# Kernel tuning notes

Hardware: AMD Instinct MI355X
Metric: run time of the kernel (lower is better)

## Reference

```python
import jax, jax.numpy as jnp
import numpy as np

NUM_HEADS = 16
HEAD_DIM = 64
D_MODEL = 1024
OUTPUT_DIM = 1024


def setup_inputs() -> dict:
    key = jax.random.key(0)
    ks = jax.random.split(key, 11)
    B, S, H = 2, 2048, D_MODEL
    inner = NUM_HEADS * HEAD_DIM
    s = 0.02
    return {
        "query": jax.random.normal(ks[0], (B, S, H), jnp.float32),
        "key": jax.random.normal(ks[1], (B, S, H), jnp.float32),
        "value": jax.random.normal(ks[2], (B, S, H), jnp.float32),
        "Wq": jax.random.normal(ks[3], (H, inner), jnp.float32) * s,
        "bq": jnp.zeros((inner,), jnp.float32),
        "Wk": jax.random.normal(ks[4], (H, inner), jnp.float32) * s,
        "bk": jnp.zeros((inner,), jnp.float32),
        "Wv": jax.random.normal(ks[5], (H, inner), jnp.float32) * s,
        "bv": jnp.zeros((inner,), jnp.float32),
        "Wo": jax.random.normal(ks[6], (inner, OUTPUT_DIM), jnp.float32) * s,
        "bo": jnp.zeros((OUTPUT_DIM,), jnp.float32),
    }


def reference(query, key, value, Wq, bq, Wk, bk, Wv, bv, Wo, bo):
    B, Sq, _ = query.shape
    Sk = key.shape[1]
    nh, dh = NUM_HEADS, HEAD_DIM
    # projections -> [B, S, nh, dh]
    Q = (query @ Wq + bq).reshape(B, Sq, nh, dh)
    K = (key @ Wk + bk).reshape(B, Sk, nh, dh)
    V = (value @ Wv + bv).reshape(B, Sk, nh, dh)
    # scores [B, nh, Sq, Sk]
    scores = jnp.einsum("bqhd,bkhd->bhqk", Q, K) / jnp.sqrt(jnp.float32(dh))
    attn = jax.nn.softmax(scores, axis=-1)
    out = jnp.einsum("bhqk,bkhd->bqhd", attn, V).reshape(B, Sq, nh * dh)
    return out @ Wo + bo
```

## Files before the change

### kernel.cpp

```cpp
#include <hip/hip_runtime.h>
#include <math.h>

typedef __attribute__((ext_vector_type(8))) short short8;
typedef __attribute__((ext_vector_type(4))) short short4v;
typedef __attribute__((ext_vector_type(4))) float f32x4;
typedef __attribute__((ext_vector_type(2))) float f32x2;

#if __has_builtin(__builtin_amdgcn_mfma_f32_16x16x16bf16_1k)
#define HAVE_MFMA16 1
#else
#define HAVE_MFMA16 0
#endif

__device__ __forceinline__ short f2bf(float f) {
  union { float f; unsigned u; } x; x.f = f;
  unsigned r = x.u + 0x7fffu + ((x.u >> 16) & 1u);
  return (short)(r >> 16);
}
#if __has_builtin(__builtin_amdgcn_cvt_pk_bf16_f32)
typedef __attribute__((ext_vector_type(2))) __bf16 bf16x2;
__device__ __forceinline__ unsigned pack_bf(float a, float b) {
  union { bf16x2 v; unsigned u; } t;
  t.v = __builtin_amdgcn_cvt_pk_bf16_f32(a, b);
  return t.u;
}
#else
__device__ __forceinline__ unsigned pack_bf(float a, float b) {
  union { float f; unsigned u; } x, y; x.f = a; y.f = b;
  unsigned ra = x.u + 0x7fffu + ((x.u >> 16) & 1u);
  unsigned rb = y.u + 0x7fffu + ((y.u >> 16) & 1u);
  return (ra >> 16) | (rb & 0xffff0000u);
}
#endif
__device__ __forceinline__ float fast_exp2(float x) {
#if __has_builtin(__builtin_amdgcn_exp2f)
  return __builtin_amdgcn_exp2f(x);
#else
  return exp2f(x);
#endif
}
union U4S8 { unsigned u[4]; short8 s; };
union U2S4 { unsigned u[2]; short4v s; };

__device__ __forceinline__ void async16(const short* g, short* lds_uniform) {
  __builtin_amdgcn_global_load_lds(
      (const __attribute__((address_space(1))) void*)g,
      (__attribute__((address_space(3))) void*)lds_uniform, 16, 0, 0);
}

__global__ __launch_bounds__(256) void wconv(
    const float* __restrict__ W0, const float* __restrict__ W1,
    const float* __restrict__ W2, const float* __restrict__ W3,
    short* __restrict__ T0, short* __restrict__ T1,
    short* __restrict__ T2, short* __restrict__ T3) {
  const float* W; short* T;
  switch (blockIdx.z) {
    case 0: W = W0; T = T0; break;
    case 1: W = W1; T = T1; break;
    case 2: W = W2; T = T2; break;
    default: W = W3; T = T3; break;
  }
  __shared__ __align__(16) short t[64][72];
  const int tid = threadIdx.x;
  const int x0 = blockIdx.x * 64, y0 = blockIdx.y * 64;
  {
    int rr = tid >> 2, cc = (tid & 3) * 16;
    const float* p = W + (size_t)(x0 + rr) * 1024 + y0 + cc;
    f32x4 v[4];
    v[0] = *(const f32x4*)(p + 0);  v[1] = *(const f32x4*)(p + 4);
    v[2] = *(const f32x4*)(p + 8);  v[3] = *(const f32x4*)(p + 12);
#pragma unroll
    for (int i = 0; i < 4; ++i)
#pragma unroll
      for (int j = 0; j < 4; ++j)
        t[cc + 4 * i + j][rr] = f2bf(v[i][j]);
  }
  __syncthreads();
  {
    int nr = tid >> 2, kc = (tid & 3) * 16;
    short* q = T + (size_t)(y0 + nr) * 1024 + x0 + kc;
    *(short8*)q       = *(const short8*)&t[nr][kc];
    *(short8*)(q + 8) = *(const short8*)&t[nr][kc + 8];
  }
}

__global__ __launch_bounds__(256) void aconv(
    const float* __restrict__ X0, const float* __restrict__ X1, const float* __restrict__ X2,
    short* __restrict__ Y0, short* __restrict__ Y1, short* __restrict__ Y2) {
  const float* X; short* Y;
  switch (blockIdx.z) {
    case 0: X = X0; Y = Y0; break;
    case 1: X = X1; Y = Y1; break;
    default: X = X2; Y = Y2; break;
  }
  size_t idx = ((size_t)blockIdx.x * 256 + threadIdx.x) * 16;
  f32x4 v0 = *(const f32x4*)(X + idx + 0);
  f32x4 v1 = *(const f32x4*)(X + idx + 4);
  f32x4 v2 = *(const f32x4*)(X + idx + 8);
  f32x4 v3 = *(const f32x4*)(X + idx + 12);
  U4S8 a, b;
  a.u[0] = pack_bf(v0[0], v0[1]); a.u[1] = pack_bf(v0[2], v0[3]);
  a.u[2] = pack_bf(v1[0], v1[1]); a.u[3] = pack_bf(v1[2], v1[3]);
  b.u[0] = pack_bf(v2[0], v2[1]); b.u[1] = pack_bf(v2[2], v2[3]);
  b.u[2] = pack_bf(v3[0], v3[1]); b.u[3] = pack_bf(v3[2], v3[3]);
  *(short8*)(Y + idx) = a.s;
  *(short8*)(Y + idx + 8) = b.s;
}

template <bool OUT_F32, int BM>
__global__ __launch_bounds__(256) void gemm_async(
    const short* __restrict__ A0, const short* __restrict__ A1, const short* __restrict__ A2,
    const short* __restrict__ B0, const short* __restrict__ B1, const short* __restrict__ B2,
    const float* __restrict__ b0, const float* __restrict__ b1, const float* __restrict__ b2,
    void* __restrict__ C0, void* __restrict__ C1, void* __restrict__ C2,
    float s0, float s1, float s2, int M, int N, int K) {
  const int z = blockIdx.z;
  const short* A    = z == 0 ? A0 : (z == 1 ? A1 : A2);
  const short* B    = z == 0 ? B0 : (z == 1 ? B1 : B2);
  const float* bias = z == 0 ? b0 : (z == 1 ? b1 : b2);
  void*        Cv   = z == 0 ? C0 : (z == 1 ? C1 : C2);
  const float  cs   = z == 0 ? s0 : (z == 1 ? s1 : s2);

  constexpr int MF = BM / 32;
  constexpr int AJ = BM / 64;
  __shared__ __align__(16) short As[BM * 32];
  __shared__ __align__(16) short Bs[128 * 32];
  const int tid = threadIdx.x;
  const int l = tid & 63, w = tid >> 6;
  const int lr = l & 15, lq = l >> 4;
  const int lin = blockIdx.x + (int)gridDim.x * blockIdx.y;
  const int ny = (int)gridDim.y;
  const int yb = lin % ny, xb = lin / ny;
  const int m0 = yb * BM, n0 = xb * 128;
  const int wm = (w >> 1) * (BM / 2), wn = (w & 1) * 64;
  f32x4 acc[MF][4] = {};

  const int lrow = l >> 2, lcol = (l & 3) * 8;
  const short* aptr[AJ];
  short* alds[AJ];
#pragma unroll
  for (int j = 0; j < AJ; ++j) {
    int chunk = w * AJ + j;
    aptr[j] = A + (size_t)(m0 + chunk * 16 + lrow) * K + lcol;
    alds[j] = &As[chunk * 512];
  }
  const short* bptr[2];
  short* blds[2];
#pragma unroll
  for (int j = 0; j < 2; ++j) {
    int chunk = w * 2 + j;
    bptr[j] = B + (size_t)(n0 + chunk * 16 + lrow) * K + lcol;
    blds[j] = &Bs[chunk * 512];
  }

  const int KT = K >> 5;
  for (int kt = 0; kt < KT; ++kt) {
    const int k0 = kt * 32;
    __syncthreads();
#pragma unroll
    for (int j = 0; j < AJ; ++j) async16(aptr[j] + k0, alds[j]);
#pragma unroll
    for (int j = 0; j < 2; ++j) async16(bptr[j] + k0, blds[j]);
    __syncthreads();

    short8 af[MF], bfr[4];
#pragma unroll
    for (int i = 0; i < MF; ++i)
      af[i] = *(const short8*)&As[(wm + i * 16 + lr) * 32 + lq * 8];
#pragma unroll
    for (int i = 0; i < 4; ++i)
      bfr[i] = *(const short8*)&Bs[(wn + i * 16 + lr) * 32 + lq * 8];
#pragma unroll
    for (int mi = 0; mi < MF; ++mi)
#pragma unroll
      for (int ni = 0; ni < 4; ++ni)
        acc[mi][ni] = __builtin_amdgcn_mfma_f32_16x16x32_bf16(af[mi], bfr[ni], acc[mi][ni], 0, 0, 0);
  }

#pragma unroll
  for (int ni = 0; ni < 4; ++ni) {
    int gn = n0 + wn + ni * 16 + lr;
    float bv = bias[gn];
#pragma unroll
    for (int mi = 0; mi < MF; ++mi) {
      int gm = m0 + wm + mi * 16 + lq * 4;
#pragma unroll
      for (int r = 0; r < 4; ++r) {
        float val = (acc[mi][ni][r] + bv) * cs;
        if constexpr (OUT_F32)
          ((float*)Cv)[(size_t)(gm + r) * N + gn] = val;
        else
          ((short*)Cv)[(size_t)(gm + r) * N + gn] = f2bf(val);
      }
    }
  }
}

template <bool A_IS_F32, bool B_IS_BF16, bool OUT_F32, int BM>
__global__ __launch_bounds__(256) void gemm_bias(
    const void* __restrict__ A0, const void* __restrict__ A1, const void* __restrict__ A2,
    const void* __restrict__ B0, const void* __restrict__ B1, const void* __restrict__ B2,
    const float* __restrict__ b0, const float* __restrict__ b1, const float* __restrict__ b2,
    void* __restrict__ C0, void* __restrict__ C1, void* __restrict__ C2,
    float s0, float s1, float s2, int M, int N, int K) {
  const int z = blockIdx.z;
  const void*  Av   = z == 0 ? A0 : (z == 1 ? A1 : A2);
  const void*  Bv   = z == 0 ? B0 : (z == 1 ? B1 : B2);
  const float* bias = z == 0 ? b0 : (z == 1 ? b1 : b2);
  void*        Cv   = z == 0 ? C0 : (z == 1 ? C1 : C2);
  const float  cs   = z == 0 ? s0 : (z == 1 ? s1 : s2);

  constexpr int MF = BM / 32;
  __shared__ __align__(16) short As[BM * 40];
  __shared__ __align__(16) short Bs[128 * 40];
  const int tid = threadIdx.x;
  const int l = tid & 63, w = tid >> 6;
  const int lr = l & 15, lq = l >> 4;
  const int lin = blockIdx.x + (int)gridDim.x * blockIdx.y;
  const int ny = (int)gridDim.y;
  const int yb = lin % ny, xb = lin / ny;
  const int m0 = yb * BM, n0 = xb * 128;
  const int wm = (w >> 1) * (BM / 2), wn = (w & 1) * 64;
  f32x4 acc[MF][4] = {};

  constexpr int TPR = 256 / BM;
  const int ar = tid / TPR, ac = (tid % TPR) * (32 / TPR);
  const int br = tid >> 1, bcc = (tid & 1) * 16;
  const int dp = tid & 63, kb = tid >> 6;

  f32x4 avf[MF];
  short8 avb[BM / 64 > 0 ? BM / 64 : 1];
  short8 bvb[2];
  f32x2 bvf[8];

  auto load_regs = [&](int k0) {
    if constexpr (A_IS_F32) {
      const float* Ap = (const float*)Av + (size_t)(m0 + ar) * K + k0 + ac;
#pragma unroll
      for (int i = 0; i < MF; ++i) avf[i] = *(const f32x4*)(Ap + 4 * i);
    } else {
      const short* Ap = (const short*)Av + (size_t)(m0 + ar) * K + k0 + ac;
#pragma unroll
      for (int i = 0; i < BM / 64; ++i) avb[i] = *(const short8*)(Ap + 8 * i);
    }
    if constexpr (B_IS_BF16) {
      const short* Bp = (const short*)Bv + (size_t)(n0 + br) * K + k0 + bcc;
      bvb[0] = *(const short8*)(Bp + 0);
      bvb[1] = *(const short8*)(Bp + 8);
    } else {
      const float* Bp = (const float*)Bv + (size_t)(k0 + kb * 8) * N + n0 + 2 * dp;
#pragma unroll
      for (int i = 0; i < 4; ++i) {
        bvf[2 * i]     = *(const f32x2*)(Bp + (size_t)(2 * i) * N);
        bvf[2 * i + 1] = *(const f32x2*)(Bp + (size_t)(2 * i + 1) * N);
      }
    }
  };
  auto write_lds = [&]() {
    if constexpr (A_IS_F32) {
#pragma unroll
      for (int j = 0; j < MF / 2; ++j) {
        U4S8 p;
        p.u[0] = pack_bf(avf[2 * j][0], avf[2 * j][1]);
        p.u[1] = pack_bf(avf[2 * j][2], avf[2 * j][3]);
        p.u[2] = pack_bf(avf[2 * j + 1][0], avf[2 * j + 1][1]);
        p.u[3] = pack_bf(avf[2 * j + 1][2], avf[2 * j + 1][3]);
        *(short8*)&As[ar * 40 + ac + 8 * j] = p.s;
      }
    } else {
#pragma unroll
      for (int j = 0; j < BM / 64; ++j)
        *(short8*)&As[ar * 40 + ac + 8 * j] = avb[j];
    }
    if constexpr (B_IS_BF16) {
      *(short8*)&Bs[br * 40 + bcc] = bvb[0];
      *(short8*)&Bs[br * 40 + bcc + 8] = bvb[1];
    } else {
      U4S8 lo, hi;
#pragma unroll
      for (int i = 0; i < 4; ++i) {
        lo.u[i] = pack_bf(bvf[2 * i][0], bvf[2 * i + 1][0]);
        hi.u[i] = pack_bf(bvf[2 * i][1], bvf[2 * i + 1][1]);
      }
      *(short8*)&Bs[(2 * dp) * 40 + kb * 8] = lo.s;
      *(short8*)&Bs[(2 * dp + 1) * 40 + kb * 8] = hi.s;
    }
  };

  load_regs(0);
  const int KT = K >> 5;
  for (int kt = 0; kt < KT; ++kt) {
    write_lds();
    __syncthreads();
    if (kt + 1 < KT) load_regs((kt + 1) * 32);

    short8 af[MF], bfr[4];
#pragma unroll
    for (int i = 0; i < MF; ++i)
      af[i] = *(const short8*)&As[(wm + i * 16 + lr) * 40 + lq * 8];
#pragma unroll
    for (int i = 0; i < 4; ++i)
      bfr[i] = *(const short8*)&Bs[(wn + i * 16 + lr) * 40 + lq * 8];
#pragma unroll
    for (int mi = 0; mi < MF; ++mi)
#pragma unroll
      for (int ni = 0; ni < 4; ++ni)
        acc[mi][ni] = __builtin_amdgcn_mfma_f32_16x16x32_bf16(af[mi], bfr[ni], acc[mi][ni], 0, 0, 0);
    __syncthreads();
  }

#pragma unroll
  for (int ni = 0; ni < 4; ++ni) {
    int gn = n0 + wn + ni * 16 + lr;
    float bv = bias[gn];
#pragma unroll
    for (int mi = 0; mi < MF; ++mi) {
      int gm = m0 + wm + mi * 16 + lq * 4;
#pragma unroll
      for (int r = 0; r < 4; ++r) {
        float val = (acc[mi][ni][r] + bv) * cs;
        if constexpr (OUT_F32)
          ((float*)Cv)[(size_t)(gm + r) * N + gn] = val;
        else
          ((short*)Cv)[(size_t)(gm + r) * N + gn] = f2bf(val);
      }
    }
  }
}

__global__ __launch_bounds__(256) void attn128db(
    const short* __restrict__ Q, const short* __restrict__ K,
    const short* __restrict__ V, short* __restrict__ ctx) {
  __shared__ __align__(16) short Ks[2][64][72];
  __shared__ __align__(16) short Vt[2][64][72];
#if !HAVE_MFMA16
  __shared__ __align__(16) short Ps2[4][32][68];
#endif
  const int tid = threadIdx.x, l = tid & 63, w = tid >> 6;
  const int lr = l & 15, lq = l >> 4;
  const int lin = blockIdx.x + 16 * blockIdx.y;
  const int h = lin & 15, qblk = lin >> 4;
  const int b = blockIdx.z, q0 = qblk * 128;
  const size_t bh = (size_t)b * 2048 * 1024 + (size_t)h * 64;
  const short* Kg = K + bh;
  const short* Vg = V + bh;

  short8 qb[2][2];
#pragma unroll
  for (int qf = 0; qf < 2; ++qf)
#pragma unroll
    for (int ks = 0; ks < 2; ++ks)
      qb[qf][ks] = *(const short8*)&Q[bh + (size_t)(q0 + w * 32 + qf * 16 + lr) * 1024 + ks * 32 + lq * 8];

  f32x4 accO[4][2] = {};
  float lpart[2] = {0.f, 0.f};

  const int kr = tid >> 2, kc = (tid & 3) * 16;
  const int vdp = tid & 31, vkb = tid >> 5;
  const int vswz = ((vkb + (vdp >> 2)) & 7) * 8;

  short8 kv0, kv1;
  unsigned vu[8];
  auto load_kv = [&](int kt) {
    const short* Kp = &Kg[(size_t)(kt * 64 + kr) * 1024 + kc];
    kv0 = *(const short8*)(Kp + 0);
    kv1 = *(const short8*)(Kp + 8);
#pragma unroll
    for (int i = 0; i < 8; ++i)
      vu[i] = *(const unsigned*)&Vg[(size_t)(kt * 64 + vkb * 8 + i) * 1024 + vdp * 2];
  };
  auto write_kv = [&](int buf) {
    *(short8*)&Ks[buf][kr][kc] = kv0;
    *(short8*)&Ks[buf][kr][kc + 8] = kv1;
    U4S8 lo, hi;
#pragma unroll
    for (int j = 0; j < 4; ++j) {
      lo.u[j] = (vu[2 * j] & 0xffffu) | (vu[2 * j + 1] << 16);
      hi.u[j] = (vu[2 * j] >> 16) | (vu[2 * j + 1] & 0xffff0000u);
    }
    *(short8*)&Vt[buf][2 * vdp][vswz] = lo.s;
    *(short8*)&Vt[buf][2 * vdp + 1][vswz] = hi.s;
  };

  load_kv(0);
  for (int kt = 0; kt < 32; ++kt) {
    const int buf = kt & 1;
    write_kv(buf);
    __syncthreads();
    if (kt + 1 < 32) load_kv(kt + 1);

    short8 ka[4][2];
#pragma unroll
    for (int ni = 0; ni < 4; ++ni)
#pragma unroll
      for (int ks = 0; ks < 2; ++ks)
        ka[ni][ks] = *(const short8*)&Ks[buf][ni * 16 + lr][ks * 32 + lq * 8];
    f32x4 s[4][2] = {};
#pragma unroll
    for (int ni = 0; ni < 4; ++ni)
#pragma unroll
      for (int qf = 0; qf < 2; ++qf) {
        s[ni][qf] = __builtin_amdgcn_mfma_f32_16x16x32_bf16(ka[ni][0], qb[qf][0], s[ni][qf], 0, 0, 0);
        s[ni][qf] = __builtin_amdgcn_mfma_f32_16x16x32_bf16(ka[ni][1], qb[qf][1], s[ni][qf], 0, 0, 0);
      }

    unsigned pk[4][2][2];
#pragma unroll
    for (int ni = 0; ni < 4; ++ni)
#pragma unroll
      for (int qf = 0; qf < 2; ++qf) {
        float p0 = fast_exp2(s[ni][qf][0]);
        float p1 = fast_exp2(s[ni][qf][1]);
        float p2 = fast_exp2(s[ni][qf][2]);
        float p3 = fast_exp2(s[ni][qf][3]);
        lpart[qf] += (p0 + p1) + (p2 + p3);
        pk[ni][qf][0] = pack_bf(p0, p1);
        pk[ni][qf][1] = pack_bf(p2, p3);
      }

#if HAVE_MFMA16
#pragma unroll
    for (int di = 0; di < 4; ++di) {
      const int dR = di * 16 + lr;
      const int ud = 2 * di + (lr >> 3);
#pragma unroll
      for (int ni = 0; ni < 4; ++ni) {
        const int pb = ((2 * ni + (lq >> 1) + ud) & 7) * 8 + (lq & 1) * 4;
        short4v vb = *(const short4v*)&Vt[buf][dR][pb];
#pragma unroll
        for (int qf = 0; qf < 2; ++qf) {
          U2S4 a; a.u[0] = pk[ni][qf][0]; a.u[1] = pk[ni][qf][1];
          accO[di][qf] = __builtin_amdgcn_mfma_f32_16x16x16bf16_1k(a.s, vb, accO[di][qf], 0, 0, 0);
        }
      }
    }
#else
#pragma unroll
    for (int ni = 0; ni < 4; ++ni)
#pragma unroll
      for (int qf = 0; qf < 2; ++qf) {
        unsigned* dst = (unsigned*)&Ps2[w][qf * 16 + lr][16 * ni + 4 * lq];
        dst[0] = pk[ni][qf][0];
        dst[1] = pk[ni][qf][1];
      }
#pragma unroll
    for (int ks = 0; ks < 2; ++ks)
#pragma unroll
      for (int qf = 0; qf < 2; ++qf) {
        const short* src = &Ps2[w][qf * 16 + lr][32 * ks + 8 * lq];
        U4S8 a;
        a.u[0] = ((const unsigned*)src)[0]; a.u[1] = ((const unsigned*)src)[1];
        a.u[2] = ((const unsigned*)src)[2]; a.u[3] = ((const unsigned*)src)[3];
#pragma unroll
        for (int di = 0; di < 4; ++di) {
          const int dR = di * 16 + lr;
          const int ud = 2 * di + (lr >> 3);
          const int pb = ((4 * ks + lq + ud) & 7) * 8;
          short8 vb = *(const short8*)&Vt[buf][dR][pb];
          accO[di][qf] = __builtin_amdgcn_mfma_f32_16x16x32_bf16(a.s, vb, accO[di][qf], 0, 0, 0);
        }
      }
#endif
  }

#pragma unroll
  for (int qf = 0; qf < 2; ++qf) {
    lpart[qf] += __shfl_xor(lpart[qf], 16, 64);
    lpart[qf] += __shfl_xor(lpart[qf], 32, 64);
  }
  float inv[2] = {1.0f / lpart[0], 1.0f / lpart[1]};
  float ir[2][4];
#pragma unroll
  for (int qf = 0; qf < 2; ++qf)
#pragma unroll
    for (int r = 0; r < 4; ++r)
      ir[qf][r] = __shfl(inv[qf], 4 * lq + r, 64);

#pragma unroll
  for (int qf = 0; qf < 2; ++qf)
#pragma unroll
    for (int r = 0; r < 4; ++r) {
      size_t row = bh + (size_t)(q0 + w * 32 + qf * 16 + 4 * lq + r) * 1024;
#pragma unroll
      for (int di = 0; di < 4; ++di)
        ctx[row + di * 16 + lr] = f2bf(accO[di][qf][r] * ir[qf][r]);
    }
}

extern "C" void kernel_launch(void* const* d_in, const int* in_sizes, int n_in,
                              void* d_out, int out_size, void* d_ws, size_t ws_size,
                              hipStream_t stream) {
  const void*  query = d_in[0];
  const void*  key   = d_in[1];
  const void*  value = d_in[2];
  const float* Wq = (const float*)d_in[3];
  const float* bq = (const float*)d_in[4];
  const float* Wk = (const float*)d_in[5];
  const float* bk = (const float*)d_in[6];
  const float* Wv = (const float*)d_in[7];
  const float* bv = (const float*)d_in[8];
  const float* Wo = (const float*)d_in[9];
  const float* bo = (const float*)d_in[10];

  short* ws = (short*)d_ws;
  const size_t MT = 4096ull * 1024ull;
  const size_t WSZ = 1024ull * 1024ull;
  const float qscale = 0.125f * 1.4426950408889634f;

  short* Qb = ws;
  short* Vb = ws + MT;
  short* Kb = (short*)d_out;

  const bool turbo = ws_size >= (4 * MT + 4 * WSZ) * sizeof(short);

  if (turbo) {
    short* Qcv = ws + 2 * MT;
    short* Vcv = ws + 3 * MT;
    short* Kcv = (short*)d_out + MT;
    short* WqT = ws + 4 * MT;
    short* WkT = WqT + WSZ;
    short* WvT = WqT + 2 * WSZ;
    short* WoT = WqT + 3 * WSZ;

    wconv<<<dim3(16, 16, 4), 256, 0, stream>>>(Wq, Wk, Wv, Wo, WqT, WkT, WvT, WoT);
    aconv<<<dim3(1024, 1, 3), 256, 0, stream>>>(
        (const float*)query, (const float*)key, (const float*)value, Qcv, Kcv, Vcv);
    gemm_async<false, 128><<<dim3(8, 32, 3), 256, 0, stream>>>(
        Qcv, Kcv, Vcv, WqT, WkT, WvT, bq, bk, bv, Qb, Kb, Vb,
        qscale, 1.0f, 1.0f, 4096, 1024, 1024);
    attn128db<<<dim3(16, 16, 2), 256, 0, stream>>>(Qb, Kb, Vb, Qb);
    gemm_async<true, 64><<<dim3(8, 64, 1), 256, 0, stream>>>(
        Qb, Qb, Qb, WoT, WoT, WoT, bo, bo, bo, d_out, d_out, d_out,
        1.0f, 1.0f, 1.0f, 4096, 1024, 1024);
    return;
  }

  const bool roomy = ws_size >= (2 * MT + 4 * WSZ) * sizeof(short);
  short *WqT, *WkT, *WvT, *WoT;
  if (roomy) {
    short* base = ws + 2 * MT;
    WqT = base; WkT = base + WSZ; WvT = base + 2 * WSZ; WoT = base + 3 * WSZ;
  } else {
    short* tail = (short*)d_out + MT;
    WqT = tail; WkT = tail + WSZ; WvT = tail + 2 * WSZ; WoT = nullptr;
  }

  wconv<<<dim3(16, 16, roomy ? 4 : 3), 256, 0, stream>>>(
      Wq, Wk, Wv, Wo, WqT, WkT, WvT, roomy ? WoT : WvT);

  gemm_bias<true, true, false, 128><<<dim3(8, 32, 3), 256, 0, stream>>>(
      query, key, value, WqT, WkT, WvT, bq, bk, bv, Qb, Kb, Vb,
      qscale, 1.0f, 1.0f, 4096, 1024, 1024);

  attn128db<<<dim3(16, 16, 2), 256, 0, stream>>>(Qb, Kb, Vb, Qb);

  if (roomy)
    gemm_bias<false, true, true, 64><<<dim3(8, 64, 1), 256, 0, stream>>>(
        Qb, Qb, Qb, WoT, WoT, WoT, bo, bo, bo, d_out, d_out, d_out,
        1.0f, 1.0f, 1.0f, 4096, 1024, 1024);
  else
    gemm_bias<false, false, true, 64><<<dim3(8, 64, 1), 256, 0, stream>>>(
        Qb, Qb, Qb, Wo, Wo, Wo, bo, bo, bo, d_out, d_out, d_out,
        1.0f, 1.0f, 1.0f, 4096, 1024, 1024);
}
```

Measured before the change: 238.9 us.

## Split attention over key halves with merge kernel; double-buffer GEMM LDS tiles

The attention kernel now optionally splits the key sequence into two halves across extra blocks, writing unnormalized partial outputs and row sums that a new merge kernel combines and normalizes. This doubles the block count to better fill the GPU's compute units, at the cost of an extra kernel launch and extra memory traffic for the partials. Separately, the async GEMM now double-buffers its LDS tiles, prefetching the next K-slice while computing the current one and removing one barrier per iteration. The softmax appears to use no running max, so summing the two halves' exp-sums directly is consistent. Partials are stored in bf16, which adds some rounding.

```diff
diff --git a/kernel.cpp b/kernel.cpp
--- a/kernel.cpp
+++ b/kernel.cpp
@@ -16,6 +16,11 @@
   union { float f; unsigned u; } x; x.f = f;
   unsigned r = x.u + 0x7fffu + ((x.u >> 16) & 1u);
   return (short)(r >> 16);
+}
+__device__ __forceinline__ float bf2f(short u) {
+  union { unsigned u; float f; } x;
+  x.u = ((unsigned)(unsigned short)u) << 16;
+  return x.f;
 }
 #if __has_builtin(__builtin_amdgcn_cvt_pk_bf16_f32)
 typedef __attribute__((ext_vector_type(2))) __bf16 bf16x2;
@@ -123,8 +128,8 @@
 
   constexpr int MF = BM / 32;
   constexpr int AJ = BM / 64;
-  __shared__ __align__(16) short As[BM * 32];
-  __shared__ __align__(16) short Bs[128 * 32];
+  __shared__ __align__(16) short As[2][BM * 32];
+  __shared__ __align__(16) short Bs[2][128 * 32];
   const int tid = threadIdx.x;
   const int l = tid & 63, w = tid >> 6;
   const int lr = l & 15, lq = l >> 4;
@@ -142,7 +147,7 @@
   for (int j = 0; j < AJ; ++j) {
     int chunk = w * AJ + j;
     aptr[j] = A + (size_t)(m0 + chunk * 16 + lrow) * K + lcol;
-    alds[j] = &As[chunk * 512];
+    alds[j] = &As[0][chunk * 512];
   }
   const short* bptr[2];
   short* blds[2];
@@ -150,26 +155,39 @@
   for (int j = 0; j < 2; ++j) {
     int chunk = w * 2 + j;
     bptr[j] = B + (size_t)(n0 + chunk * 16 + lrow) * K + lcol;
-    blds[j] = &Bs[chunk * 512];
-  }
+    blds[j] = &Bs[0][chunk * 512];
+  }
+
+#pragma unroll
+  for (int j = 0; j < AJ; ++j) async16(aptr[j], alds[j]);
+#pragma unroll
+  for (int j = 0; j < 2; ++j) async16(bptr[j], blds[j]);
 
   const int KT = K >> 5;
   for (int kt = 0; kt < KT; ++kt) {
-    const int k0 = kt * 32;
+    const int buf = kt & 1;
     __syncthreads();
-#pragma unroll
-    for (int j = 0; j < AJ; ++j) async16(aptr[j] + k0, alds[j]);
-#pragma unroll
-    for (int j = 0; j < 2; ++j) async16(bptr[j] + k0, blds[j]);
-    __syncthreads();
+    if (kt + 1 < KT) {
+      const int k1 = (kt + 1) * 32;
+      const int off = (buf ^ 1) ? 0 : 1;
+      short* at = (buf ^ 1) ? (short*)&As[1][0] : (short*)&As[0][0];
+      short* bt = (buf ^ 1) ? (short*)&Bs[1][0] : (short*)&Bs[0][0];
+      (void)off;
+#pragma unroll
+      for (int j = 0; j < AJ; ++j)
+        async16(aptr[j] + k1, at + (alds[j] - &As[0][0]));
+#pragma unroll
+      for (int j = 0; j < 2; ++j)
+        async16(bptr[j] + k1, bt + (blds[j] - &Bs[0][0]));
+    }
 
     short8 af[MF], bfr[4];
 #pragma unroll
     for (int i = 0; i < MF; ++i)
-      af[i] = *(const short8*)&As[(wm + i * 16 + lr) * 32 + lq * 8];
+      af[i] = *(const short8*)&As[buf][(wm + i * 16 + lr) * 32 + lq * 8];
 #pragma unroll
     for (int i = 0; i < 4; ++i)
-      bfr[i] = *(const short8*)&Bs[(wn + i * 16 + lr) * 32 + lq * 8];
+      bfr[i] = *(const short8*)&Bs[buf][(wn + i * 16 + lr) * 32 + lq * 8];
 #pragma unroll
     for (int mi = 0; mi < MF; ++mi)
 #pragma unroll
@@ -328,9 +346,11 @@
   }
 }
 
+template <bool SPLIT>
 __global__ __launch_bounds__(256) void attn128db(
     const short* __restrict__ Q, const short* __restrict__ K,
-    const short* __restrict__ V, short* __restrict__ ctx) {
+    const short* __restrict__ V, short* __restrict__ ctx,
+    short* __restrict__ O0, short* __restrict__ O1, float* __restrict__ lbuf) {
   __shared__ __align__(16) short Ks[2][64][72];
   __shared__ __align__(16) short Vt[2][64][72];
 #if !HAVE_MFMA16
@@ -340,7 +360,12 @@
   const int lr = l & 15, lq = l >> 4;
   const int lin = blockIdx.x + 16 * blockIdx.y;
   const int h = lin & 15, qblk = lin >> 4;
-  const int b = blockIdx.z, q0 = qblk * 128;
+  const int z = blockIdx.z;
+  const int b = SPLIT ? (z >> 1) : z;
+  const int half = SPLIT ? (z & 1) : 0;
+  const int kt0 = SPLIT ? half * 16 : 0;
+  const int KTN = SPLIT ? 16 : 32;
+  const int q0 = qblk * 128;
   const size_t bh = (size_t)b * 2048 * 1024 + (size_t)h * 64;
   const short* Kg = K + bh;
   const short* Vg = V + bh;
@@ -382,12 +407,12 @@
     *(short8*)&Vt[buf][2 * vdp + 1][vswz] = hi.s;
   };
 
-  load_kv(0);
-  for (int kt = 0; kt < 32; ++kt) {
-    const int buf = kt & 1;
+  load_kv(kt0);
+  for (int i = 0; i < KTN; ++i) {
+    const int buf = i & 1;
     write_kv(buf);
     __syncthreads();
-    if (kt + 1 < 32) load_kv(kt + 1);
+    if (i + 1 < KTN) load_kv(kt0 + i + 1);
 
     short8 ka[4][2];
 #pragma unroll
@@ -468,23 +493,63 @@
     lpart[qf] += __shfl_xor(lpart[qf], 16, 64);
     lpart[qf] += __shfl_xor(lpart[qf], 32, 64);
   }
-  float inv[2] = {1.0f / lpart[0], 1.0f / lpart[1]};
-  float ir[2][4];
-#pragma unroll
-  for (int qf = 0; qf < 2; ++qf)
-#pragma unroll
-    for (int r = 0; r < 4; ++r)
-      ir[qf][r] = __shfl(inv[qf], 4 * lq + r, 64);
-
-#pragma unroll
-  for (int qf = 0; qf < 2; ++qf)
-#pragma unroll
-    for (int r = 0; r < 4; ++r) {
-      size_t row = bh + (size_t)(q0 + w * 32 + qf * 16 + 4 * lq + r) * 1024;
-#pragma unroll
-      for (int di = 0; di < 4; ++di)
-        ctx[row + di * 16 + lr] = f2bf(accO[di][qf][r] * ir[qf][r]);
-    }
+
+  if constexpr (SPLIT) {
+    short* Op = half ? O1 : O0;
+    if (lq == 0) {
+      float* lb = lbuf + ((size_t)((half * 2 + b) * 16 + h)) * 2048;
+      lb[q0 + w * 32 + lr] = lpart[0];
+      lb[q0 + w * 32 + 16 + lr] = lpart[1];
+    }
+#pragma unroll
+    for (int qf = 0; qf < 2; ++qf)
+#pragma unroll
+      for (int r = 0; r < 4; ++r) {
+        size_t row = bh + (size_t)(q0 + w * 32 + qf * 16 + 4 * lq + r) * 1024;
+#pragma unroll
+        for (int di = 0; di < 4; ++di)
+          Op[row + di * 16 + lr] = f2bf(accO[di][qf][r]);
+      }
+  } else {
+    float inv[2] = {1.0f / lpart[0], 1.0f / lpart[1]};
+    float ir[2][4];
+#pragma unroll
+    for (int qf = 0; qf < 2; ++qf)
+#pragma unroll
+      for (int r = 0; r < 4; ++r)
+        ir[qf][r] = __shfl(inv[qf], 4 * lq + r, 64);
+#pragma unroll
+    for (int qf = 0; qf < 2; ++qf)
+#pragma unroll
+      for (int r = 0; r < 4; ++r) {
+        size_t row = bh + (size_t)(q0 + w * 32 + qf * 16 + 4 * lq + r) * 1024;
+#pragma unroll
+        for (int di = 0; di < 4; ++di)
+          ctx[row + di * 16 + lr] = f2bf(accO[di][qf][r] * ir[qf][r]);
+      }
+  }
+}
+
+__global__ __launch_bounds__(256) void merge_attn(
+    const short* __restrict__ O0, const short* __restrict__ O1,
+    const float* __restrict__ lbuf, short* __restrict__ ctx) {
+  size_t i = ((size_t)blockIdx.x * 256 + threadIdx.x) * 8;
+  int rq = (int)(i >> 10);
+  int b = rq >> 11, q = rq & 2047;
+  int h = ((int)i & 1023) >> 6;
+  float l0 = lbuf[((size_t)((0 + b) * 16 + h)) * 2048 + q];
+  float l1 = lbuf[((size_t)((2 + b) * 16 + h)) * 2048 + q];
+  float inv = 1.0f / (l0 + l1);
+  short8 a = *(const short8*)(O0 + i);
+  short8 c = *(const short8*)(O1 + i);
+  U4S8 o;
+#pragma unroll
+  for (int j = 0; j < 4; ++j) {
+    float x0 = (bf2f(a[2 * j]) + bf2f(c[2 * j])) * inv;
+    float x1 = (bf2f(a[2 * j + 1]) + bf2f(c[2 * j + 1])) * inv;
+    o.u[j] = pack_bf(x0, x1);
+  }
+  *(short8*)(ctx + i) = o.s;
 }
 
 extern "C" void kernel_launch(void* const* d_in, const int* in_sizes, int n_in,
@@ -521,6 +586,7 @@
     short* WkT = WqT + WSZ;
     short* WvT = WqT + 2 * WSZ;
     short* WoT = WqT + 3 * WSZ;
+    float* lbuf = (float*)Kcv;
 
     wconv<<<dim3(16, 16, 4), 256, 0, stream>>>(Wq, Wk, Wv, Wo, WqT, WkT, WvT, WoT);
     aconv<<<dim3(1024, 1, 3), 256, 0, stream>>>(
@@ -528,7 +594,9 @@
     gemm_async<false, 128><<<dim3(8, 32, 3), 256, 0, stream>>>(
         Qcv, Kcv, Vcv, WqT, WkT, WvT, bq, bk, bv, Qb, Kb, Vb,
         qscale, 1.0f, 1.0f, 4096, 1024, 1024);
-    attn128db<<<dim3(16, 16, 2), 256, 0, stream>>>(Qb, Kb, Vb, Qb);
+    attn128db<true><<<dim3(16, 16, 4), 256, 0, stream>>>(
+        Qb, Kb, Vb, nullptr, Qcv, Vcv, lbuf);
+    merge_attn<<<dim3(2048), 256, 0, stream>>>(Qcv, Vcv, lbuf, Qb);
     gemm_async<true, 64><<<dim3(8, 64, 1), 256, 0, stream>>>(
         Qb, Qb, Qb, WoT, WoT, WoT, bo, bo, bo, d_out, d_out, d_out,
         1.0f, 1.0f, 1.0f, 4096, 1024, 1024);
@@ -552,7 +620,8 @@
       query, key, value, WqT, WkT, WvT, bq, bk, bv, Qb, Kb, Vb,
       qscale, 1.0f, 1.0f, 4096, 1024, 1024);
 
-  attn128db<<<dim3(16, 16, 2), 256, 0, stream>>>(Qb, Kb, Vb, Qb);
+  attn128db<false><<<dim3(16, 16, 2), 256, 0, stream>>>(
+      Qb, Kb, Vb, Qb, nullptr, nullptr, nullptr);
 
   if (roomy)
     gemm_bias<false, true, true, 64><<<dim3(8, 64, 1), 256, 0, stream>>>(
```

After: 234.1 us. -2.0%, faster.
